# Performance work log

Hardware: AMD Instinct MI355X
Metric: run time of the kernel (lower is better)

The kernel has to match this reference:

```python
import jax, jax.numpy as jnp
import numpy as np

B, C, D, J = 8, 2048, 128, 128

def setup_inputs() -> dict:
    key = jax.random.key(0)
    ks = jax.random.split(key, 24)
    s = 0.02
    inp = {
        "operation_features": jax.random.normal(ks[0], (B, C, D), jnp.float32),
        "relations": jax.random.randint(ks[1], (B, C - 2, 2), 0, C, jnp.int64),
        "begins_idx": jax.random.randint(ks[2], (B, J), 0, C, jnp.int64),
        "ends_idx": jax.random.randint(ks[3], (B, J), 0, C, jnp.int64),
        "same_type_mask": (jax.random.uniform(ks[4], (B, C, C)) > 0.5).astype(jnp.float32),
        # BeginEndEncoder
        "W_begin": jax.random.normal(ks[5], (D, D), jnp.float32) * s,
        "b_begin": jnp.zeros((D,), jnp.float32),
        "W_end": jax.random.normal(ks[6], (D, D), jnp.float32) * s,
        "b_end": jnp.zeros((D,), jnp.float32),
        # OperationTimeRelationEncoder.mix: Linear(3D -> D)
        "W_mix3": jax.random.normal(ks[7], (3 * D, D), jnp.float32) * s,
        "b_mix3": jnp.zeros((D,), jnp.float32),
        # SelfAttention (hidden_dim = D)
        "W_qkv": jax.random.normal(ks[8], (D, 3 * D), jnp.float32) * s,
        "b_qkv": jnp.zeros((3 * D,), jnp.float32),
        "w_score": jax.random.normal(ks[9], (2 * D,), jnp.float32) * s,
        "b_score": jnp.zeros((), jnp.float32),
        "W_out": jax.random.normal(ks[10], (D, D), jnp.float32) * s,
        "b_out": jnp.zeros((D,), jnp.float32),
        # block mix: Linear(2D -> D)
        "W_mix2": jax.random.normal(ks[11], (2 * D, D), jnp.float32) * s,
        "b_mix2": jnp.zeros((D,), jnp.float32),
    }
    return inp

def _gather_ops(ops, idx):
    # ops: [B,C,D], idx: [B,M] -> [B,M,D]  (torch.gather along dim 1 with expanded index)
    Bb, _, Dd = ops.shape
    M = idx.shape[1]
    return jnp.take_along_axis(ops, jnp.broadcast_to(idx[:, :, None], (Bb, M, Dd)), axis=1)

def reference(operation_features, relations, begins_idx, ends_idx, same_type_mask,
              W_begin, b_begin, W_end, b_end, W_mix3, b_mix3,
              W_qkv, b_qkv, w_score, b_score, W_out, b_out, W_mix2, b_mix2):
    ops = operation_features
    Dd = ops.shape[-1]
    # --- OperationTimeRelationEncoder ---
    pred = _gather_ops(ops, relations[..., 0])      # [B,C-2,D]
    succ = _gather_ops(ops, relations[..., 1])      # [B,C-2,D]
    concated = jnp.concatenate([ops[:, :-2, :], pred, succ], axis=-1)  # [B,C-2,3D]
    mixed = concated @ W_mix3 + b_mix3              # [B,C-2,D]
    begin_f = _gather_ops(ops, begins_idx) @ W_begin + b_begin  # [B,J,D]
    end_f = _gather_ops(ops, ends_idx) @ W_end + b_end
    begin = jnp.mean(begin_f, axis=1)               # [B,D]
    end = jnp.mean(end_f, axis=1)
    seq = jnp.concatenate([mixed, begin[:, None, :], end[:, None, :]], axis=1)  # [B,C,D]
    # --- SelfAttention (GAT-style additive score, decomposed to avoid CxCx2h blowup) ---
    qkv = ops @ W_qkv + b_qkv                       # [B,C,3D]
    q, k, v = jnp.split(qkv, 3, axis=-1)
    sq = q @ w_score[:Dd]                           # [B,C]  q_i . w_q
    sk = k @ w_score[Dd:]                           # [B,C]  k_j . w_k
    scores = jax.nn.leaky_relu(sq[:, :, None] + sk[:, None, :] + b_score)  # [B,C,C]
    attn = jax.nn.softmax(scores * same_type_mask, axis=-1)                # multiplicative mask, as in torch
    weighted = jnp.einsum('bij,bjd->bid', attn, v)  # [B,C,D]
    same_type = weighted @ W_out + b_out            # [B,C,D]
    # --- final mix ---
    return jnp.concatenate([seq, same_type], axis=-1) @ W_mix2 + b_mix2  # [B,C,D]
```

## Files before the change

### kernel.cpp

```cpp
#include <hip/hip_runtime.h>
#include <cstddef>

typedef __bf16 bf16;
typedef __bf16 bf16x4 __attribute__((ext_vector_type(4)));
typedef __bf16 bf16x8 __attribute__((ext_vector_type(8)));
typedef float  f32x4  __attribute__((ext_vector_type(4)));

#define MFMA16(a, b, c) __builtin_amdgcn_mfma_f32_16x16x32_bf16((a), (b), (c), 0, 0, 0)

#define BB 8
#define CC 2048
#define DD 128
#define JJN 128

#define WS_PK    ((size_t)0)
#define WS_OPS16 ((size_t)8388608)
#define WS_SQF   ((size_t)12582912)
#define WS_SKF   ((size_t)12648448)
#define WS_G1T   ((size_t)12713984)
#define WS_G2T   ((size_t)12746752)
#define WS_G3T   ((size_t)12779520)
#define WS_WCT   ((size_t)12812288)
#define WS_GBT   ((size_t)12845056)
#define WS_GET   ((size_t)12877824)
#define WS_UQK   ((size_t)12910592)
#define WS_BBM   ((size_t)12911104)
#define WS_BBB   ((size_t)12911616)
#define WS_BBE   ((size_t)12912128)
#define WS_SC    ((size_t)12912640)
#define WS_WCN   ((size_t)12913152)
#define WS_GBN   ((size_t)12945920)
#define WS_GEN   ((size_t)12978688)
#define WS_MB    ((size_t)13011456)
#define WS_MEANV ((size_t)17205760)

__global__ __launch_bounds__(256) void k_prepcast(
    const float* __restrict__ ops, bf16* __restrict__ ops16,
    const float* __restrict__ mask, const int* __restrict__ begins,
    const int* __restrict__ ends,
    const float* __restrict__ Wmix3, const float* __restrict__ Wmix2,
    const float* __restrict__ Wout,  const float* __restrict__ Wbegin,
    const float* __restrict__ Wend,  const float* __restrict__ Wqkv,
    const float* __restrict__ bqkv,  const float* __restrict__ wscore,
    const float* __restrict__ bscore,const float* __restrict__ bmix3,
    const float* __restrict__ bout,  const float* __restrict__ bmix2,
    const float* __restrict__ bbegin,const float* __restrict__ bend,
    bf16* __restrict__ G1T, bf16* __restrict__ G2T, bf16* __restrict__ G3T,
    bf16* __restrict__ WCT, bf16* __restrict__ GBT, bf16* __restrict__ GET,
    bf16* __restrict__ WCN, bf16* __restrict__ GBN, bf16* __restrict__ GEN,
    bf16* __restrict__ uqk, float* __restrict__ BBM, float* __restrict__ BBB,
    float* __restrict__ BBE, float* __restrict__ sc,
    unsigned char* __restrict__ MBITS, float* __restrict__ MEANV)
{
    __shared__ bf16  LshT[128 * 132];
    __shared__ float Rsh[128 * 8];
    int wg = blockIdx.x;
    int t  = threadIdx.x;

    if (wg == 0) {
        for (int half = 0; half < 2; ++half) {
            #pragma unroll
            for (int pass = 0; pass < 16; ++pass) {
                int idx = pass * 256 + t;
                int d   = idx >> 5;
                int e0  = (idx & 31) * 4;
                f32x4 v = *(const f32x4*)(Wqkv + d*384 + half*128 + e0);
                #pragma unroll
                for (int jj = 0; jj < 4; ++jj)
                    LshT[(e0 + jj)*132 + d] = (bf16)v[jj];
            }
            if (t < 32) {
                f32x4 wv = *(const f32x4*)(wscore + half*128 + t*4);
                #pragma unroll
                for (int jj = 0; jj < 4; ++jj) Rsh[t*4 + jj] = wv[jj];
            }
            __syncthreads();
            if (t < 128) {
                float s = 0.f;
                for (int e = 0; e < 128; ++e)
                    s += (float)LshT[e*132 + t] * Rsh[e];
                uqk[half*128 + t] = (bf16)s;
            }
            __syncthreads();
        }
        float bm = 0.f, bb_ = 0.f, be_ = 0.f, bon = 0.f;
        for (int half = 0; half < 2; ++half) {
            #pragma unroll
            for (int pass = 0; pass < 16; ++pass) {
                int idx = pass * 256 + t;
                int f   = idx >> 5;
                int e0  = (idx & 31) * 4;
                f32x4 v = *(const f32x4*)(Wmix2 + (size_t)(half*128 + f)*128 + e0);
                #pragma unroll
                for (int jj = 0; jj < 4; ++jj)
                    LshT[f*132 + e0 + jj] = (bf16)v[jj];
            }
            if (t < 32) {
                if (half == 0) {
                    f32x4 v0 = *(const f32x4*)(bmix3  + t*4);
                    f32x4 v1 = *(const f32x4*)(bbegin + t*4);
                    f32x4 v2 = *(const f32x4*)(bend   + t*4);
                    #pragma unroll
                    for (int jj = 0; jj < 4; ++jj) {
                        Rsh[t*4 + jj]       = v0[jj];
                        Rsh[128 + t*4 + jj] = v1[jj];
                        Rsh[256 + t*4 + jj] = v2[jj];
                    }
                } else {
                    f32x4 v3 = *(const f32x4*)(bout + t*4);
                    #pragma unroll
                    for (int jj = 0; jj < 4; ++jj) Rsh[t*4 + jj] = v3[jj];
                }
            }
            __syncthreads();
            if (t < 128) {
                if (half == 0) {
                    for (int f = 0; f < 128; ++f) {
                        float wv = (float)LshT[f*132 + t];
                        bm  += Rsh[f]       * wv;
                        bb_ += Rsh[128 + f] * wv;
                        be_ += Rsh[256 + f] * wv;
                    }
                } else {
                    for (int f = 0; f < 128; ++f)
                        bon += Rsh[f] * (float)LshT[f*132 + t];
                }
            }
            __syncthreads();
        }
        if (t < 128) {
            float bm2 = bmix2[t];
            BBM[t] = bm  + bon + bm2;
            BBB[t] = bb_ + bon + bm2;
            BBE[t] = be_ + bon + bm2;
        }
        if (t >= 128) {
            int e2 = t - 128;
            Rsh[512 + e2] = bqkv[e2]       * wscore[e2];
            Rsh[640 + e2] = bqkv[128 + e2] * wscore[128 + e2];
        }
        __syncthreads();
        if (t == 0) {
            float cq = 0.f, ck = 0.f;
            for (int e2 = 0; e2 < 128; ++e2) {
                cq += Rsh[512 + e2];
                ck += Rsh[640 + e2];
            }
            sc[0] = cq + bscore[0];
            sc[1] = ck;
        }
        return;
    }
    if (wg <= 16) {
        int task = wg - 1;
        int b2 = task >> 1, which = task & 1;
        const int* idxp = which ? (ends + b2 * JJN) : (begins + b2 * JJN);
        int* ish = (int*)Rsh;
        if (t < JJN) ish[t] = idxp[t];
        __syncthreads();
        int d = t & 127, half = t >> 7;
        const float* opsb = ops + (size_t)b2 * CC * DD;
        float s = 0.f;
        #pragma unroll 8
        for (int j = 0; j < 64; ++j) {
            int r = ish[half * 64 + j];
            s += opsb[(size_t)r * DD + d];
        }
        float* fsh = Rsh + 256;
        fsh[half * 128 + d] = s;
        __syncthreads();
        if (t < 128)
            MEANV[task * 128 + t] = (fsh[t] + fsh[128 + t]) * (1.0f / (float)JJN);
        return;
    }
    if (wg <= 2064) {
        int p = wg - 17;
        size_t base = (size_t)p * 16384;
        const float* mp = mask + base;
        unsigned char* ob = MBITS + (base >> 3);
        #pragma unroll
        for (int k = 0; k < 8; ++k) {
            size_t fo = (size_t)k * 2048 + (size_t)t * 8;
            f32x4 a = __builtin_nontemporal_load((const f32x4*)(mp + fo));
            f32x4 c = __builtin_nontemporal_load((const f32x4*)(mp + fo + 4));
            unsigned byte = 0;
            #pragma unroll
            for (int e = 0; e < 4; ++e) {
                byte |= (a[e] != 0.f ? 1u : 0u) << e;
                byte |= (c[e] != 0.f ? 1u : 0u) << (4 + e);
            }
            ob[k * 256 + t] = (unsigned char)byte;
        }
        return;
    }
    if (wg <= 2160) {
        int id  = wg - 2065;
        int mat = id >> 4, sub = id & 15;
        const float* L; const float* R; bf16* O; bf16* O2;
        switch (mat) {
            case 0: L = Wmix3;           R = Wmix2;           O = G1T; O2 = nullptr; break;
            case 1: L = Wmix3 + 128*128; R = Wmix2;           O = G2T; O2 = nullptr; break;
            case 2: L = Wmix3 + 256*128; R = Wmix2;           O = G3T; O2 = nullptr; break;
            case 3: L = Wout;            R = Wmix2 + 128*128; O = WCT; O2 = WCN; break;
            case 4: L = Wbegin;          R = Wmix2;           O = GBT; O2 = GBN; break;
            default:L = Wend;            R = Wmix2;           O = GET; O2 = GEN; break;
        }
        int e0 = sub * 8;
        #pragma unroll
        for (int pass = 0; pass < 16; ++pass) {
            int idx = pass * 256 + t;
            int d   = idx >> 5;
            int f0  = (idx & 31) * 4;
            f32x4 v = *(const f32x4*)(L + d * 128 + f0);
            #pragma unroll
            for (int jj = 0; jj < 4; ++jj)
                LshT[(f0 + jj) * 132 + d] = (bf16)v[jj];
        }
        #pragma unroll
        for (int pass = 0; pass < 4; ++pass) {
            int idx = pass * 256 + t;
            int f   = idx >> 3;
            int ee  = idx & 7;
            Rsh[f * 8 + ee] = R[f * 128 + e0 + ee];
        }
        __syncthreads();
        int ee = t >> 5;
        int e  = e0 + ee;
        int d0 = (t & 31) * 4;
        float s[4] = {0.f, 0.f, 0.f, 0.f};
        for (int f = 0; f < 128; ++f) {
            bf16x4 lv = *(const bf16x4*)&LshT[f * 132 + d0];
            float rv = Rsh[f * 8 + ee];
            #pragma unroll
            for (int dd = 0; dd < 4; ++dd)
                s[dd] += (float)lv[dd] * rv;
        }
        #pragma unroll
        for (int dd = 0; dd < 4; ++dd) {
            O[e * 128 + d0 + dd] = (bf16)s[dd];
            if (O2) O2[(d0 + dd) * 128 + e] = (bf16)s[dd];
        }
        return;
    }
    size_t i = (size_t)(wg - 2161) * 256 + t;
    f32x4 a = *(const f32x4*)(ops + i * 8);
    f32x4 b = *(const f32x4*)(ops + i * 8 + 4);
    bf16x8 o;
    #pragma unroll
    for (int e = 0; e < 4; ++e) { o[e] = (bf16)a[e]; o[4 + e] = (bf16)b[e]; }
    *(bf16x8*)(ops16 + i * 8) = o;
}

__global__ __launch_bounds__(256) void k_v(
    const bf16* __restrict__ ops16, const float* __restrict__ Wqkv,
    const float* __restrict__ bqkv, const bf16* __restrict__ uqk,
    const float* __restrict__ sc,
    bf16* __restrict__ PK, float* __restrict__ sqf, float* __restrict__ skf)
{
    __shared__ bf16 A[144 * 136];
    int b  = blockIdx.x & 7;
    int jt = (blockIdx.x >> 3) * 64;
    int t  = threadIdx.x;
    #pragma unroll
    for (int pass = 0; pass < 16; ++pass) {
        int idx = pass * 256 + t;
        int d   = idx >> 5;
        int n0  = (idx & 31) * 4;
        f32x4 v = *(const f32x4*)(Wqkv + d*384 + 256 + n0);
        #pragma unroll
        for (int jj = 0; jj < 4; ++jj)
            A[(n0 + jj)*136 + d] = (bf16)v[jj];
    }
    {
        int row = t >> 7, col = t & 127;
        A[(128 + row)*136 + col] = uqk[row*128 + col];
    }
    for (int idx = t; idx < 14*136; idx += 256)
        A[130*136 + idx] = (bf16)0.f;
    __syncthreads();

    int lane = t & 63, w = t >> 6;
    int m = lane & 15, q = lane >> 4;
    f32x4 acc[9];
    #pragma unroll
    for (int rb = 0; rb < 9; ++rb) acc[rb] = {0.f, 0.f, 0.f, 0.f};

    const bf16* opsb = ops16 + (size_t)b * CC * DD;
    int j = jt + w*16 + m;
    #pragma unroll
    for (int kc = 0; kc < 4; ++kc) {
        bf16x8 bfr = *(const bf16x8*)(opsb + (size_t)j*DD + kc*32 + q*8);
        #pragma unroll
        for (int rb = 0; rb < 9; ++rb) {
            bf16x8 afr = *(const bf16x8*)&A[(rb*16 + m)*136 + kc*32 + q*8];
            acc[rb] = MFMA16(afr, bfr, acc[rb]);
        }
    }
    float cqb = sc[0], ckv = sc[1];
    if (q == 0) {
        sqf[b*CC + j] = acc[8][0] + cqb;
        skf[b*CC + j] = acc[8][1] + ckv;
    }
    __syncthreads();
    bf16* pack = A;
    {
        int jcl = w >> 1;
        int qv  = (w & 1) * 2 + (m >> 3);
        int ev  = m & 7;
        #pragma unroll
        for (int rb = 0; rb < 8; ++rb) {
            #pragma unroll
            for (int r = 0; r < 4; ++r) {
                float v = acc[rb][r] + bqkv[256 + rb*16 + q*4 + r];
                pack[jcl*4096 + rb*512 + qv*128 + (q*4+r)*8 + ev] = (bf16)v;
            }
        }
    }
    __syncthreads();
    bf16* pkb = PK + (size_t)b * DD * CC + (size_t)jt * 128;
    #pragma unroll
    for (int pass = 0; pass < 4; ++pass) {
        int lidx = pass * 256 + t;
        *(uint4*)(pkb + (size_t)lidx * 8) = *(const uint4*)&pack[lidx * 8];
    }
}

__device__ __forceinline__ void load_vb(const bf16* __restrict__ pkb, int jc,
                                        int q, int m, bf16x8 vb[8])
{
    #pragma unroll
    for (int nb = 0; nb < 8; ++nb)
        vb[nb] = *(const bf16x8*)(pkb + ((size_t)(((jc*8 + nb)*4 + q)*16 + m)) * 8);
}

__device__ __forceinline__ void substep(const float* __restrict__ skw,
    unsigned mbyte, int jo, float sq,
    const bf16x8 vb[8], float& lsum, f32x4 acc[8])
{
    f32x4 s0 = *(const f32x4*)(skw + jo);
    f32x4 s1 = *(const f32x4*)(skw + jo + 4);
    float sks[8] = {s0[0], s0[1], s0[2], s0[3], s1[0], s1[1], s1[2], s1[3]};
    bf16x8 a;
    #pragma unroll
    for (int e = 0; e < 8; ++e) {
        float tv = sq + sks[e];
        float lr = fmaxf(tv, 0.01f * tv);
        float pm = (float)((mbyte >> e) & 1u);
        float p  = __expf(lr * pm);
        lsum += p;
        a[e] = (bf16)p;
    }
    #pragma unroll
    for (int nb = 0; nb < 8; ++nb)
        acc[nb] = MFMA16(a, vb[nb], acc[nb]);
}

__global__ __launch_bounds__(256) void k_attepi(
    const unsigned char* __restrict__ MBITS, const bf16* __restrict__ PK,
    const float* __restrict__ sqf, const float* __restrict__ skf,
    const bf16* __restrict__ ops16, const int* __restrict__ relations,
    const bf16* __restrict__ G1T, const bf16* __restrict__ G2T,
    const bf16* __restrict__ G3T, const bf16* __restrict__ WCT,
    const bf16* __restrict__ GBN, const bf16* __restrict__ GEN,
    const bf16* __restrict__ WCN,
    const float* __restrict__ BBM, const float* __restrict__ BBB,
    const float* __restrict__ BBE, const float* __restrict__ MEANV,
    float* __restrict__ out)
{
    __shared__ __align__(16) char smem[52224];
    int t    = threadIdx.x;
    int lane = t & 63, w = t >> 6;
    int b    = blockIdx.x & 7;
    int i0   = (blockIdx.x >> 3) << 5;
    int m = lane & 15, q = lane >> 4;

    unsigned char* Lb  = (unsigned char*)smem;
    float*         skw = (float*)(smem + 8704 + w * 2048);

    {
        int row = t >> 3, seg = t & 7;
        const uint4* src = (const uint4*)(MBITS
            + ((size_t)(b * CC + i0 + row)) * 256 + seg * 32);
        uint4 v0 = src[0], v1 = src[1];
        *(uint4*)(Lb + row * 272 + seg * 32)      = v0;
        *(uint4*)(Lb + row * 272 + seg * 32 + 16) = v1;
    }
    {
        const float* src = skf + b * CC + w * 512;
        *(f32x4*)(skw + lane * 4)       = *(const f32x4*)(src + lane * 4);
        *(f32x4*)(skw + 256 + lane * 4) = *(const f32x4*)(src + 256 + lane * 4);
    }
    float sq0 = sqf[b * CC + i0 + m];
    float sq1 = sqf[b * CC + i0 + 16 + m];
    const bf16* pkb = PK + (size_t)b * DD * CC;
    int jc0 = w * 16;

    f32x4 acc0[8], acc1[8];
    #pragma unroll
    for (int nb = 0; nb < 8; ++nb) {
        acc0[nb] = {0.f, 0.f, 0.f, 0.f};
        acc1[nb] = {0.f, 0.f, 0.f, 0.f};
    }
    float lsum0 = 0.f, lsum1 = 0.f;
    __syncthreads();

    bf16x8 vbA[8], vbB[8];
    load_vb(pkb, jc0, q, m, vbA);
    #pragma unroll
    for (int c = 0; c < 16; c += 2) {
        load_vb(pkb, jc0 + c + 1, q, m, vbB);
        {
            int bo = w * 64 + c * 4 + q;
            unsigned mb0 = Lb[m * 272 + bo];
            unsigned mb1 = Lb[(16 + m) * 272 + bo];
            substep(skw, mb0, c * 32 + q * 8, sq0, vbA, lsum0, acc0);
            substep(skw, mb1, c * 32 + q * 8, sq1, vbA, lsum1, acc1);
        }
        if (c + 2 < 16) load_vb(pkb, jc0 + c + 2, q, m, vbA);
        {
            int bo = w * 64 + (c + 1) * 4 + q;
            unsigned mb0 = Lb[m * 272 + bo];
            unsigned mb1 = Lb[(16 + m) * 272 + bo];
            substep(skw, mb0, (c + 1) * 32 + q * 8, sq0, vbB, lsum0, acc0);
            substep(skw, mb1, (c + 1) * 32 + q * 8, sq1, vbB, lsum1, acc1);
        }
    }

    __syncthreads();
    float* Osh  = (float*)(smem + 8704);
    float* Lsh  = (float*)(smem + 42496);
    bf16*  Obuf = (bf16*)(smem + 43520);
    #pragma unroll
    for (int tile = 0; tile < 2; ++tile) {
        float ls = tile ? lsum1 : lsum0;
        ls += __shfl_xor(ls, 16, 64);
        ls += __shfl_xor(ls, 32, 64);
        if (q == 0) Lsh[w * 16 + m] = ls;
        const f32x4* acc = tile ? acc1 : acc0;
        #pragma unroll
        for (int nb = 0; nb < 8; ++nb)
            #pragma unroll
            for (int r = 0; r < 4; ++r)
                Osh[(w * 16 + q * 4 + r) * 132 + nb * 16 + m] = acc[nb][r];
        __syncthreads();

        int r   = t >> 4;
        int c0e = (t & 15) * 8;
        float l = Lsh[r] + Lsh[16 + r] + Lsh[32 + r] + Lsh[48 + r];
        float inv = 1.0f / l;
        bf16x8 o;
        #pragma unroll
        for (int e = 0; e < 8; ++e) {
            float s = Osh[r * 132 + c0e + e] + Osh[(16 + r) * 132 + c0e + e]
                    + Osh[(32 + r) * 132 + c0e + e] + Osh[(48 + r) * 132 + c0e + e];
            o[e] = (bf16)(s * inv);
        }
        *(bf16x8*)&Obuf[(tile * 16 + r) * 136 + c0e] = o;
        __syncthreads();
    }

    bf16* Abuf = (bf16*)smem;
    bf16* Bbuf = (bf16*)(smem + 8704);

    f32x4 eacc[2][2];
    #pragma unroll
    for (int rb = 0; rb < 2; ++rb)
        #pragma unroll
        for (int cb = 0; cb < 2; ++cb)
            eacc[rb][cb] = {0.f, 0.f, 0.f, 0.f};

    const bf16* Bsrc[4] = {G1T, G2T, G3T, WCT};
    int arow = t >> 3, ao = (t & 7) * 16;
    int brow = t >> 1, bo2 = (t & 1) * 64;
    int c = i0 + arow;

    for (int term = 0; term < 4; ++term) {
        if (term < 3) {
            const bf16* src;
            if (term == 0) src = ops16 + ((size_t)(b * CC + c)) * DD;
            else {
                int ridx = relations[((size_t)b * (CC - 2) + min(c, CC - 3)) * 2 + (term - 1)];
                src = ops16 + ((size_t)(b * CC) + ridx) * DD;
            }
            *(uint4*)&Abuf[arow * 136 + ao]     = *(const uint4*)(src + ao);
            *(uint4*)&Abuf[arow * 136 + ao + 8] = *(const uint4*)(src + ao + 8);
        }
        const uint4* bs = (const uint4*)(Bsrc[term] + brow * 128 + bo2);
        uint4* bd = (uint4*)&Bbuf[brow * 136 + bo2];
        #pragma unroll
        for (int ii = 0; ii < 8; ++ii) bd[ii] = bs[ii];
        __syncthreads();

        const bf16* Asrc = (term == 3) ? Obuf : Abuf;
        #pragma unroll
        for (int kc = 0; kc < 4; ++kc) {
            bf16x8 bfr[2];
            #pragma unroll
            for (int cb = 0; cb < 2; ++cb)
                bfr[cb] = *(const bf16x8*)&Bbuf[(w * 32 + cb * 16 + m) * 136 + kc * 32 + q * 8];
            #pragma unroll
            for (int rb = 0; rb < 2; ++rb) {
                bf16x8 afr = *(const bf16x8*)&Asrc[(rb * 16 + m) * 136 + kc * 32 + q * 8];
                eacc[rb][0] = MFMA16(afr, bfr[0], eacc[rb][0]);
                eacc[rb][1] = MFMA16(afr, bfr[1], eacc[rb][1]);
            }
        }
        __syncthreads();
    }
    #pragma unroll
    for (int cb = 0; cb < 2; ++cb) {
        int col = w * 32 + cb * 16 + m;
        float bias = BBM[col];
        #pragma unroll
        for (int rb = 0; rb < 2; ++rb) {
            #pragma unroll
            for (int r = 0; r < 4; ++r) {
                int cg = i0 + rb * 16 + q * 4 + r;
                if (cg < CC - 2)
                    out[((size_t)(b * CC) + cg) * DD + col] = eacc[rb][cb][r] + bias;
            }
        }
    }

    if (i0 == CC - 32) {
        __syncthreads();
        float* mv2 = (float*)smem;
        int grp = t >> 7, tl = t & 127;
        mv2[grp * 128 + tl] = MEANV[((size_t)b * 2 + grp) * 128 + tl];
        __syncthreads();
        int which = grp;
        const bf16* G    = which ? GEN : GBN;
        const float* Bv  = which ? BBE : BBB;
        const bf16* orow = Obuf + (30 + which) * 136;
        float a = Bv[tl];
        const float* mv = mv2 + grp * 128;
        for (int d = 0; d < 128; ++d) {
            a += mv[d] * (float)G[d * 128 + tl];
            a += (float)orow[d] * (float)WCN[d * 128 + tl];
        }
        out[((size_t)b * CC + (CC - 2 + which)) * DD + tl] = a;
    }
}

extern "C" void kernel_launch(void* const* d_in, const int* in_sizes, int n_in,
                              void* d_out, int out_size, void* d_ws, size_t ws_size,
                              hipStream_t stream)
{
    const float* ops      = (const float*)d_in[0];
    const int*  relations = (const int*)d_in[1];
    const int*  begins    = (const int*)d_in[2];
    const int*  ends      = (const int*)d_in[3];
    const float* mask     = (const float*)d_in[4];
    const float* Wbegin   = (const float*)d_in[5];
    const float* bbegin   = (const float*)d_in[6];
    const float* Wend     = (const float*)d_in[7];
    const float* bend     = (const float*)d_in[8];
    const float* Wmix3    = (const float*)d_in[9];
    const float* bmix3    = (const float*)d_in[10];
    const float* Wqkv     = (const float*)d_in[11];
    const float* bqkv     = (const float*)d_in[12];
    const float* wscore   = (const float*)d_in[13];
    const float* bscore   = (const float*)d_in[14];
    const float* Wout     = (const float*)d_in[15];
    const float* bout     = (const float*)d_in[16];
    const float* Wmix2    = (const float*)d_in[17];
    const float* bmix2    = (const float*)d_in[18];
    float* outp = (float*)d_out;

    char* ws = (char*)d_ws;
    bf16*  PK    = (bf16*)(ws + WS_PK);
    bf16*  OPS16 = (bf16*)(ws + WS_OPS16);
    float* sqf   = (float*)(ws + WS_SQF);
    float* skf   = (float*)(ws + WS_SKF);
    bf16*  G1T   = (bf16*)(ws + WS_G1T);
    bf16*  G2T   = (bf16*)(ws + WS_G2T);
    bf16*  G3T   = (bf16*)(ws + WS_G3T);
    bf16*  WCT   = (bf16*)(ws + WS_WCT);
    bf16*  GBT   = (bf16*)(ws + WS_GBT);
    bf16*  GET   = (bf16*)(ws + WS_GET);
    bf16*  WCN   = (bf16*)(ws + WS_WCN);
    bf16*  GBN   = (bf16*)(ws + WS_GBN);
    bf16*  GEN   = (bf16*)(ws + WS_GEN);
    bf16*  UQK   = (bf16*)(ws + WS_UQK);
    float* BBM   = (float*)(ws + WS_BBM);
    float* BBB   = (float*)(ws + WS_BBB);
    float* BBE   = (float*)(ws + WS_BBE);
    float* SC    = (float*)(ws + WS_SC);
    unsigned char* MBITS = (unsigned char*)(ws + WS_MB);
    float* MEANV = (float*)(ws + WS_MEANV);

    k_prepcast<<<dim3(3185), dim3(256), 0, stream>>>(
        ops, OPS16, mask, begins, ends,
        Wmix3, Wmix2, Wout, Wbegin, Wend, Wqkv, bqkv, wscore, bscore,
        bmix3, bout, bmix2, bbegin, bend,
        G1T, G2T, G3T, WCT, GBT, GET, WCN, GBN, GEN,
        UQK, BBM, BBB, BBE, SC, MBITS, MEANV);

    k_v<<<dim3(256), dim3(256), 0, stream>>>(
        OPS16, Wqkv, bqkv, UQK, SC, PK, sqf, skf);

    k_attepi<<<dim3(512), dim3(256), 0, stream>>>(
        MBITS, PK, sqf, skf, OPS16, relations,
        G1T, G2T, G3T, WCT, GBN, GEN, WCN, BBM, BBB, BBE, MEANV, outp);
}
```

Before: 279.8 us.

## Double attention-epilogue block to 512 threads, splitting key range across eight waves

The fused attention+epilogue kernel now launches 512 threads per block: eight waves each handle 256 keys instead of four waves handling 512. The manual double-buffered V loads are replaced by a simple per-chunk load, and the partial accumulators from waves 4-7 are added into shared memory in a second pass. The epilogue GEMM gives each wave 16 output columns. The aim is more latency hiding and a shorter serial key loop per wave, at the cost of extra reduction syncs and a launch-bounds hint that may limit registers.

```diff
diff --git a/kernel.cpp b/kernel.cpp
--- a/kernel.cpp
+++ b/kernel.cpp
@@ -333,29 +333,7 @@
         vb[nb] = *(const bf16x8*)(pkb + ((size_t)(((jc*8 + nb)*4 + q)*16 + m)) * 8);
 }
 
-__device__ __forceinline__ void substep(const float* __restrict__ skw,
-    unsigned mbyte, int jo, float sq,
-    const bf16x8 vb[8], float& lsum, f32x4 acc[8])
-{
-    f32x4 s0 = *(const f32x4*)(skw + jo);
-    f32x4 s1 = *(const f32x4*)(skw + jo + 4);
-    float sks[8] = {s0[0], s0[1], s0[2], s0[3], s1[0], s1[1], s1[2], s1[3]};
-    bf16x8 a;
-    #pragma unroll
-    for (int e = 0; e < 8; ++e) {
-        float tv = sq + sks[e];
-        float lr = fmaxf(tv, 0.01f * tv);
-        float pm = (float)((mbyte >> e) & 1u);
-        float p  = __expf(lr * pm);
-        lsum += p;
-        a[e] = (bf16)p;
-    }
-    #pragma unroll
-    for (int nb = 0; nb < 8; ++nb)
-        acc[nb] = MFMA16(a, vb[nb], acc[nb]);
-}
-
-__global__ __launch_bounds__(256) void k_attepi(
+__global__ __launch_bounds__(512, 4) void k_attepi(
     const unsigned char* __restrict__ MBITS, const bf16* __restrict__ PK,
     const float* __restrict__ sqf, const float* __restrict__ skf,
     const bf16* __restrict__ ops16, const int* __restrict__ relations,
@@ -375,25 +353,19 @@
     int m = lane & 15, q = lane >> 4;
 
     unsigned char* Lb  = (unsigned char*)smem;
-    float*         skw = (float*)(smem + 8704 + w * 2048);
+    float*         skw = (float*)(smem + 8704 + w * 1024);
 
     {
-        int row = t >> 3, seg = t & 7;
-        const uint4* src = (const uint4*)(MBITS
-            + ((size_t)(b * CC + i0 + row)) * 256 + seg * 32);
-        uint4 v0 = src[0], v1 = src[1];
-        *(uint4*)(Lb + row * 272 + seg * 32)      = v0;
-        *(uint4*)(Lb + row * 272 + seg * 32 + 16) = v1;
-    }
-    {
-        const float* src = skf + b * CC + w * 512;
-        *(f32x4*)(skw + lane * 4)       = *(const f32x4*)(src + lane * 4);
-        *(f32x4*)(skw + 256 + lane * 4) = *(const f32x4*)(src + 256 + lane * 4);
-    }
+        int row = t >> 4, seg = t & 15;
+        *(uint4*)(Lb + row * 272 + seg * 16) = *(const uint4*)(MBITS
+            + ((size_t)(b * CC + i0 + row)) * 256 + seg * 16);
+    }
+    *(f32x4*)(skw + lane * 4) = *(const f32x4*)(skf + b * CC + w * 256 + lane * 4);
+
     float sq0 = sqf[b * CC + i0 + m];
     float sq1 = sqf[b * CC + i0 + 16 + m];
     const bf16* pkb = PK + (size_t)b * DD * CC;
-    int jc0 = w * 16;
+    int jc0 = w * 8;
 
     f32x4 acc0[8], acc1[8];
     #pragma unroll
@@ -404,29 +376,40 @@
     float lsum0 = 0.f, lsum1 = 0.f;
     __syncthreads();
 
-    bf16x8 vbA[8], vbB[8];
-    load_vb(pkb, jc0, q, m, vbA);
-    #pragma unroll
-    for (int c = 0; c < 16; c += 2) {
-        load_vb(pkb, jc0 + c + 1, q, m, vbB);
-        {
-            int bo = w * 64 + c * 4 + q;
-            unsigned mb0 = Lb[m * 272 + bo];
-            unsigned mb1 = Lb[(16 + m) * 272 + bo];
-            substep(skw, mb0, c * 32 + q * 8, sq0, vbA, lsum0, acc0);
-            substep(skw, mb1, c * 32 + q * 8, sq1, vbA, lsum1, acc1);
-        }
-        if (c + 2 < 16) load_vb(pkb, jc0 + c + 2, q, m, vbA);
-        {
-            int bo = w * 64 + (c + 1) * 4 + q;
-            unsigned mb0 = Lb[m * 272 + bo];
-            unsigned mb1 = Lb[(16 + m) * 272 + bo];
-            substep(skw, mb0, (c + 1) * 32 + q * 8, sq0, vbB, lsum0, acc0);
-            substep(skw, mb1, (c + 1) * 32 + q * 8, sq1, vbB, lsum1, acc1);
-        }
-    }
-
+    #pragma unroll
+    for (int c = 0; c < 8; ++c) {
+        bf16x8 vb[8];
+        load_vb(pkb, jc0 + c, q, m, vb);
+        int bo = (jc0 + c) * 4 + q;
+        unsigned mb0 = Lb[m * 272 + bo];
+        unsigned mb1 = Lb[(16 + m) * 272 + bo];
+        int jo = c * 32 + q * 8;
+        f32x4 s0 = *(const f32x4*)(skw + jo);
+        f32x4 s1 = *(const f32x4*)(skw + jo + 4);
+        float sks[8] = {s0[0], s0[1], s0[2], s0[3], s1[0], s1[1], s1[2], s1[3]};
+        bf16x8 a0, a1;
+        #pragma unroll
+        for (int e = 0; e < 8; ++e) {
+            float sk = sks[e];
+            float t0 = sq0 + sk;
+            float l0 = fmaxf(t0, 0.01f * t0);
+            float p0 = __expf(l0 * (float)((mb0 >> e) & 1u));
+            lsum0 += p0;
+            a0[e] = (bf16)p0;
+            float t1 = sq1 + sk;
+            float l1 = fmaxf(t1, 0.01f * t1);
+            float p1 = __expf(l1 * (float)((mb1 >> e) & 1u));
+            lsum1 += p1;
+            a1[e] = (bf16)p1;
+        }
+        #pragma unroll
+        for (int nb = 0; nb < 8; ++nb) {
+            acc0[nb] = MFMA16(a0, vb[nb], acc0[nb]);
+            acc1[nb] = MFMA16(a1, vb[nb], acc1[nb]);
+        }
+    }
     __syncthreads();
+
     float* Osh  = (float*)(smem + 8704);
     float* Lsh  = (float*)(smem + 42496);
     bf16*  Obuf = (bf16*)(smem + 43520);
@@ -435,43 +418,52 @@
         float ls = tile ? lsum1 : lsum0;
         ls += __shfl_xor(ls, 16, 64);
         ls += __shfl_xor(ls, 32, 64);
-        if (q == 0) Lsh[w * 16 + m] = ls;
         const f32x4* acc = tile ? acc1 : acc0;
-        #pragma unroll
-        for (int nb = 0; nb < 8; ++nb)
-            #pragma unroll
-            for (int r = 0; r < 4; ++r)
-                Osh[(w * 16 + q * 4 + r) * 132 + nb * 16 + m] = acc[nb][r];
-        __syncthreads();
-
-        int r   = t >> 4;
-        int c0e = (t & 15) * 8;
-        float l = Lsh[r] + Lsh[16 + r] + Lsh[32 + r] + Lsh[48 + r];
-        float inv = 1.0f / l;
-        bf16x8 o;
-        #pragma unroll
-        for (int e = 0; e < 8; ++e) {
-            float s = Osh[r * 132 + c0e + e] + Osh[(16 + r) * 132 + c0e + e]
-                    + Osh[(32 + r) * 132 + c0e + e] + Osh[(48 + r) * 132 + c0e + e];
-            o[e] = (bf16)(s * inv);
-        }
-        *(bf16x8*)&Obuf[(tile * 16 + r) * 136 + c0e] = o;
+        if (w < 4) {
+            if (q == 0) Lsh[w*16 + m] = ls;
+            #pragma unroll
+            for (int nb = 0; nb < 8; ++nb)
+                #pragma unroll
+                for (int r = 0; r < 4; ++r)
+                    Osh[(w*16 + q*4 + r)*132 + nb*16 + m] = acc[nb][r];
+        }
+        __syncthreads();
+        if (w >= 4) {
+            if (q == 0) Lsh[(w-4)*16 + m] += ls;
+            #pragma unroll
+            for (int nb = 0; nb < 8; ++nb)
+                #pragma unroll
+                for (int r = 0; r < 4; ++r)
+                    Osh[((w-4)*16 + q*4 + r)*132 + nb*16 + m] += acc[nb][r];
+        }
+        __syncthreads();
+        if (t < 256) {
+            int r   = t >> 4;
+            int c0e = (t & 15) * 8;
+            float l = Lsh[r] + Lsh[16 + r] + Lsh[32 + r] + Lsh[48 + r];
+            float inv = 1.0f / l;
+            bf16x8 o;
+            #pragma unroll
+            for (int e = 0; e < 8; ++e) {
+                float s = Osh[r*132 + c0e + e] + Osh[(16 + r)*132 + c0e + e]
+                        + Osh[(32 + r)*132 + c0e + e] + Osh[(48 + r)*132 + c0e + e];
+                o[e] = (bf16)(s * inv);
+            }
+            *(bf16x8*)&Obuf[(tile * 16 + r) * 136 + c0e] = o;
+        }
         __syncthreads();
     }
 
     bf16* Abuf = (bf16*)smem;
     bf16* Bbuf = (bf16*)(smem + 8704);
 
-    f32x4 eacc[2][2];
-    #pragma unroll
-    for (int rb = 0; rb < 2; ++rb)
-        #pragma unroll
-        for (int cb = 0; cb < 2; ++cb)
-            eacc[rb][cb] = {0.f, 0.f, 0.f, 0.f};
+    f32x4 eacc[2];
+    eacc[0] = {0.f, 0.f, 0.f, 0.f};
+    eacc[1] = {0.f, 0.f, 0.f, 0.f};
 
     const bf16* Bsrc[4] = {G1T, G2T, G3T, WCT};
-    int arow = t >> 3, ao = (t & 7) * 16;
-    int brow = t >> 1, bo2 = (t & 1) * 64;
+    int arow = t >> 4, ao = (t & 15) * 8;
+    int brow = t >> 2, bo2 = (t & 3) * 32;
     int c = i0 + arow;
 
     for (int term = 0; term < 4; ++term) {
@@ -482,42 +474,36 @@
                 int ridx = relations[((size_t)b * (CC - 2) + min(c, CC - 3)) * 2 + (term - 1)];
                 src = ops16 + ((size_t)(b * CC) + ridx) * DD;
             }
-            *(uint4*)&Abuf[arow * 136 + ao]     = *(const uint4*)(src + ao);
-            *(uint4*)&Abuf[arow * 136 + ao + 8] = *(const uint4*)(src + ao + 8);
-        }
-        const uint4* bs = (const uint4*)(Bsrc[term] + brow * 128 + bo2);
-        uint4* bd = (uint4*)&Bbuf[brow * 136 + bo2];
-        #pragma unroll
-        for (int ii = 0; ii < 8; ++ii) bd[ii] = bs[ii];
+            *(uint4*)&Abuf[arow * 136 + ao] = *(const uint4*)(src + ao);
+        }
+        #pragma unroll
+        for (int ii = 0; ii < 4; ++ii)
+            *(uint4*)&Bbuf[brow * 136 + bo2 + ii*8] =
+                *(const uint4*)(Bsrc[term] + brow * 128 + bo2 + ii*8);
         __syncthreads();
 
         const bf16* Asrc = (term == 3) ? Obuf : Abuf;
         #pragma unroll
         for (int kc = 0; kc < 4; ++kc) {
-            bf16x8 bfr[2];
-            #pragma unroll
-            for (int cb = 0; cb < 2; ++cb)
-                bfr[cb] = *(const bf16x8*)&Bbuf[(w * 32 + cb * 16 + m) * 136 + kc * 32 + q * 8];
+            bf16x8 bfr = *(const bf16x8*)&Bbuf[(w*16 + m)*136 + kc*32 + q*8];
             #pragma unroll
             for (int rb = 0; rb < 2; ++rb) {
-                bf16x8 afr = *(const bf16x8*)&Asrc[(rb * 16 + m) * 136 + kc * 32 + q * 8];
-                eacc[rb][0] = MFMA16(afr, bfr[0], eacc[rb][0]);
-                eacc[rb][1] = MFMA16(afr, bfr[1], eacc[rb][1]);
-            }
-        }
-        __syncthreads();
-    }
-    #pragma unroll
-    for (int cb = 0; cb < 2; ++cb) {
-        int col = w * 32 + cb * 16 + m;
+                bf16x8 afr = *(const bf16x8*)&Asrc[(rb*16 + m)*136 + kc*32 + q*8];
+                eacc[rb] = MFMA16(afr, bfr, eacc[rb]);
+            }
+        }
+        __syncthreads();
+    }
+    {
+        int col = w*16 + m;
         float bias = BBM[col];
         #pragma unroll
         for (int rb = 0; rb < 2; ++rb) {
             #pragma unroll
             for (int r = 0; r < 4; ++r) {
-                int cg = i0 + rb * 16 + q * 4 + r;
+                int cg = i0 + rb*16 + q*4 + r;
                 if (cg < CC - 2)
-                    out[((size_t)(b * CC) + cg) * DD + col] = eacc[rb][cb][r] + bias;
+                    out[((size_t)(b * CC) + cg) * DD + col] = eacc[rb][r] + bias;
             }
         }
     }
@@ -525,20 +511,24 @@
     if (i0 == CC - 32) {
         __syncthreads();
         float* mv2 = (float*)smem;
-        int grp = t >> 7, tl = t & 127;
-        mv2[grp * 128 + tl] = MEANV[((size_t)b * 2 + grp) * 128 + tl];
-        __syncthreads();
-        int which = grp;
-        const bf16* G    = which ? GEN : GBN;
-        const float* Bv  = which ? BBE : BBB;
-        const bf16* orow = Obuf + (30 + which) * 136;
-        float a = Bv[tl];
-        const float* mv = mv2 + grp * 128;
-        for (int d = 0; d < 128; ++d) {
-            a += mv[d] * (float)G[d * 128 + tl];
-            a += (float)orow[d] * (float)WCN[d * 128 + tl];
-        }
-        out[((size_t)b * CC + (CC - 2 + which)) * DD + tl] = a;
+        if (t < 256)
+            mv2[(t >> 7) * 128 + (t & 127)] =
+                MEANV[((size_t)b * 2 + (t >> 7)) * 128 + (t & 127)];
+        __syncthreads();
+        if (t < 256) {
+            int grp = t >> 7, tl = t & 127;
+            int which = grp;
+            const bf16* G    = which ? GEN : GBN;
+            const float* Bv  = which ? BBE : BBB;
+            const bf16* orow = Obuf + (30 + which) * 136;
+            float a = Bv[tl];
+            const float* mv = mv2 + grp * 128;
+            for (int d = 0; d < 128; ++d) {
+                a += mv[d] * (float)G[d * 128 + tl];
+                a += (float)orow[d] * (float)WCN[d * 128 + tl];
+            }
+            out[((size_t)b * CC + (CC - 2 + which)) * DD + tl] = a;
+        }
     }
 }
 
@@ -599,7 +589,7 @@
     k_v<<<dim3(256), dim3(256), 0, stream>>>(
         OPS16, Wqkv, bqkv, UQK, SC, PK, sqf, skf);
 
-    k_attepi<<<dim3(512), dim3(256), 0, stream>>>(
+    k_attepi<<<dim3(512), dim3(512), 0, stream>>>(
         MBITS, PK, sqf, skf, OPS16, relations,
         G1T, G2T, G3T, WCT, GBN, GEN, WCN, BBM, BBB, BBE, MEANV, outp);
 }
```

After: 316.4 us. +13.1%, slower.
